# Kernel optimization log

Hardware: AMD Instinct MI355X
Metric: run time of the kernel (lower is better)

## Reference

```python
import jax, jax.numpy as jnp
import numpy as np

N, B, E, H = 16384, 16, 131072, 2
NPG = N // B  # nodes per graph
DIMS = [128, 256, 512]  # in==out channels per GAT layer


def setup_inputs() -> dict:
    key = jax.random.key(0)
    ks = iter(jax.random.split(key, 40))
    inp = {"node_feats": jax.random.normal(next(ks), (N, DIMS[0]), jnp.float32)}
    for l, d in enumerate(DIMS):
        s = 1.0 / np.sqrt(d)
        inp[f"W{l}"] = jax.random.normal(next(ks), (d, H * d), jnp.float32) * s
        inp[f"attnl{l}"] = jax.random.normal(next(ks), (H, d), jnp.float32) * 0.1
        inp[f"attnr{l}"] = jax.random.normal(next(ks), (H, d), jnp.float32) * 0.1
        inp[f"resW{l}"] = jax.random.normal(next(ks), (d, H * d), jnp.float32) * s
        inp[f"gamma{l}"] = jnp.ones((d,), jnp.float32)
        inp[f"beta{l}"] = jnp.zeros((d,), jnp.float32)
        inp[f"alpha{l}"] = jnp.ones((d,), jnp.float32)
    dst = jax.random.randint(next(ks), (E,), 0, N, jnp.int32)
    # source node sampled from the same graph as the destination
    src = (dst // NPG) * NPG + jax.random.randint(next(ks), (E,), 0, NPG, jnp.int32)
    inp["edge_src"] = src
    inp["edge_dst"] = dst
    inp["graph_ids"] = jnp.repeat(jnp.arange(B, dtype=jnp.int32), NPG)
    return inp


def _gat(x, W, al, ar, rW, src, dst, d):
    # x: [N, in]; W,rW: [in, H*d]; al,ar: [H,d]
    h = (x @ W).reshape(N, H, d)
    el = jnp.sum(h * al, -1)  # [N,H]
    er = jnp.sum(h * ar, -1)  # [N,H]
    e = jax.nn.leaky_relu(el[src] + er[dst], 0.2)  # [E,H]
    m = jax.ops.segment_max(e, dst, num_segments=N)
    ex = jnp.exp(e - m[dst])
    a = ex / jax.ops.segment_sum(ex, dst, num_segments=N)[dst]  # edge softmax
    out = jax.ops.segment_sum(h[src] * a[:, :, None], dst, num_segments=N)
    return out + (x @ rW).reshape(N, H, d)  # residual projection


def _gnorm(x, gamma, beta, alpha, eps=1e-5):
    # GraphNorm: (x - alpha*mean) / std * gamma + beta, stats over all nodes/heads
    mean = jnp.mean(x, axis=(0, 1), keepdims=True)
    sh = x - alpha * mean
    var = jnp.mean(sh * sh, axis=(0, 1), keepdims=True)
    return gamma * sh * jax.lax.rsqrt(var + eps) + beta


def reference(node_feats, W0, attnl0, attnr0, resW0, gamma0, beta0, alpha0,
              W1, attnl1, attnr1, resW1, gamma1, beta1, alpha1,
              W2, attnl2, attnr2, resW2, gamma2, beta2, alpha2,
              edge_src, edge_dst, graph_ids):
    params = [(W0, attnl0, attnr0, resW0, gamma0, beta0, alpha0),
              (W1, attnl1, attnr1, resW1, gamma1, beta1, alpha1),
              (W2, attnl2, attnr2, resW2, gamma2, beta2, alpha2)]
    counts = jax.ops.segment_sum(jnp.ones((N,), jnp.float32), graph_ids, num_segments=B)
    x = node_feats
    parts = []
    for l, d in enumerate(DIMS):
        W, al, ar, rW, g, b, a_ = params[l]
        x = _gat(x.reshape(N, -1), W, al, ar, rW, edge_src, edge_dst, d)  # [N,H,d]
        x = _gnorm(x, g, b, a_)
        x = jax.nn.leaky_relu(x, 0.01)
        nm = x.mean(1)  # [N,d] head-mean stored as 'updated_feats'
        parts.append(jax.ops.segment_sum(nm, graph_ids, num_segments=B) / counts[:, None])
    return jax.nn.leaky_relu(jnp.concatenate(parts, -1), 0.01)  # [B, 896]
```

## Files before the change

### kernel.cpp

```cpp
#include <hip/hip_runtime.h>
#include <math.h>

constexpr int NNODES  = 16384;
constexpr int NEDGES  = 131072;
constexpr int NGRAPHS = 16;

typedef short bf16x8 __attribute__((ext_vector_type(8)));
typedef short bf16x4 __attribute__((ext_vector_type(4)));
typedef float f32x4  __attribute__((ext_vector_type(4)));

__device__ __forceinline__ float leaky(float x, float s){ return x >= 0.0f ? x : s * x; }

__device__ __forceinline__ unsigned short f2bf(float f){
  unsigned u = __builtin_bit_cast(unsigned, f);
  u += 0x7FFFu + ((u >> 16) & 1u);
  return (unsigned short)(u >> 16);
}
__device__ __forceinline__ float bf2f(unsigned short u){
  unsigned x = (unsigned)u << 16; return __builtin_bit_cast(float, x);
}

__device__ __forceinline__ void gload_lds16(const unsigned short* g, unsigned short* l){
  __builtin_amdgcn_global_load_lds((const __attribute__((address_space(1))) void*)g,
                                   (__attribute__((address_space(3))) void*)l, 16, 0, 0);
}

__global__ void k_deg(const int* __restrict__ dst, int* __restrict__ deg){
  int e = blockIdx.x * 256 + threadIdx.x;
  if (e < NEDGES) atomicAdd(&deg[dst[e]], 1);
}

__global__ __launch_bounds__(1024) void k_scan(const int* __restrict__ deg,
                                               int* __restrict__ rowptr,
                                               int* __restrict__ cursor){
  __shared__ int sums[1024];
  int t = threadIdx.x;
  int loc[16];
  int s = 0;
  #pragma unroll
  for (int i = 0; i < 16; i++){ loc[i] = deg[t*16 + i]; s += loc[i]; }
  sums[t] = s; __syncthreads();
  for (int off = 1; off < 1024; off <<= 1){
    int v = (t >= off) ? sums[t - off] : 0;
    __syncthreads();
    sums[t] += v;
    __syncthreads();
  }
  int base = (t > 0) ? sums[t-1] : 0;
  #pragma unroll
  for (int i = 0; i < 16; i++){
    rowptr[t*16 + i] = base; cursor[t*16 + i] = base; base += loc[i];
  }
  if (t == 1023) rowptr[NNODES] = base;
}

__global__ void k_scatter(const int* __restrict__ src, const int* __restrict__ dst,
                          int* __restrict__ cursor, int* __restrict__ perm){
  int e = blockIdx.x * 256 + threadIdx.x;
  if (e < NEDGES){ int p = atomicAdd(&cursor[dst[e]], 1); perm[p] = src[e]; }
}

__global__ __launch_bounds__(256) void k_counts(const int* __restrict__ gid, float* __restrict__ counts){
  __shared__ int h[NGRAPHS];
  int t = threadIdx.x;
  if (t < NGRAPHS) h[t] = 0;
  __syncthreads();
  int base = blockIdx.x * 1024;
  #pragma unroll
  for (int i = 0; i < 4; i++)
    atomicAdd(&h[gid[base + t + i*256]], 1);
  __syncthreads();
  if (t < NGRAPHS && h[t] > 0) atomicAdd(&counts[t], (float)h[t]);
}

__global__ void k_cvt(const float* __restrict__ in, unsigned short* __restrict__ out, int n4){
  int i = blockIdx.x * 256 + threadIdx.x;
  if (i >= n4) return;
  float4 v = ((const float4*)in)[i];
  ushort4 o; o.x = f2bf(v.x); o.y = f2bf(v.y); o.z = f2bf(v.z); o.w = f2bf(v.w);
  ((ushort4*)out)[i] = o;
}

__global__ __launch_bounds__(256) void k_cvt_t(const float* __restrict__ W,
                                               unsigned short* __restrict__ Wt,
                                               int K, int NN){
  __shared__ float tile[32][33];
  int n0 = blockIdx.x * 32, k0 = blockIdx.y * 32;
  int tx = threadIdx.x & 31, ty = threadIdx.x >> 5;
  #pragma unroll
  for (int i = 0; i < 4; i++)
    tile[ty + i*8][tx] = W[(size_t)(k0 + ty + i*8) * NN + n0 + tx];
  __syncthreads();
  #pragma unroll
  for (int i = 0; i < 4; i++)
    Wt[(size_t)(n0 + ty + i*8) * K + k0 + tx] = f2bf(tile[tx][ty + i*8]);
}

__global__ __launch_bounds__(256) void k_gemm2(const unsigned short* __restrict__ A,
                                               const unsigned short* __restrict__ Wt,
                                               const unsigned short* __restrict__ RWt,
                                               unsigned short* __restrict__ HB,
                                               float* __restrict__ RB,
                                               int K, int NN){
  __shared__ unsigned short As[2][128 * 64];
  __shared__ unsigned short Bs[2][128 * 64];
  int t = threadIdx.x;
  int lane = t & 63, w = t >> 6;
  int nx  = gridDim.x;
  int nwg = nx * gridDim.y;
  int bid = blockIdx.x + blockIdx.y * nx;
  int wg  = (bid & 7) * (nwg >> 3) + (bid >> 3);
  int bx = wg % nx, by = wg / nx;
  int half = nx >> 1;
  bool isW = bx < half;
  const unsigned short* Bt = isW ? Wt : RWt;
  int colB = (isW ? bx : bx - half) * 128;
  int rowA = by * 128;

  int wr = (w >> 1) * 64, wc = (w & 1) * 64;
  int l16 = lane & 15, lhi = lane >> 4;
  int r8  = lane >> 3;
  int kcs = (((lane & 7) * 16) ^ (r8 << 4)) >> 1;
  f32x4 acc[4][4] = {};

  const unsigned short* Ap = A  + (size_t)(rowA) * K + kcs;
  const unsigned short* Bp = Bt + (size_t)(colB) * K + kcs;

  int nt = K >> 6;
  #pragma unroll
  for (int i = 0; i < 4; i++){
    int c = w * 4 + i;
    int row = c * 8 + r8;
    gload_lds16(Ap + (size_t)row * K, &As[0][c * 512]);
    gload_lds16(Bp + (size_t)row * K, &Bs[0][c * 512]);
  }
  __syncthreads();

  int cur = 0;
  for (int tI = 0; tI < nt; tI++){
    if (tI + 1 < nt){
      int k0n = (tI + 1) << 6;
      #pragma unroll
      for (int i = 0; i < 4; i++){
        int c = w * 4 + i;
        int row = c * 8 + r8;
        gload_lds16(Ap + (size_t)row * K + k0n, &As[cur ^ 1][c * 512]);
        gload_lds16(Bp + (size_t)row * K + k0n, &Bs[cur ^ 1][c * 512]);
      }
    }
    bf16x8 af[4][2], bfr[4][2];
    #pragma unroll
    for (int mi = 0; mi < 4; mi++){
      int row = wr + mi * 16 + l16;
      #pragma unroll
      for (int s = 0; s < 2; s++){
        int k = s * 32 + lhi * 8;
        int off = row * 128 + ((k * 2) ^ ((row & 7) << 4));
        af[mi][s] = *(const bf16x8*)((const char*)As[cur] + off);
      }
    }
    #pragma unroll
    for (int ni = 0; ni < 4; ni++){
      int row = wc + ni * 16 + l16;
      #pragma unroll
      for (int s = 0; s < 2; s++){
        int k = s * 32 + lhi * 8;
        int off = row * 128 + ((k * 2) ^ ((row & 7) << 4));
        bfr[ni][s] = *(const bf16x8*)((const char*)Bs[cur] + off);
      }
    }
    #pragma unroll
    for (int mi = 0; mi < 4; mi++)
      #pragma unroll
      for (int ni = 0; ni < 4; ni++){
        acc[mi][ni] = __builtin_amdgcn_mfma_f32_16x16x32_bf16(af[mi][0], bfr[ni][0], acc[mi][ni], 0, 0, 0);
        acc[mi][ni] = __builtin_amdgcn_mfma_f32_16x16x32_bf16(af[mi][1], bfr[ni][1], acc[mi][ni], 0, 0, 0);
      }
    __syncthreads();
    cur ^= 1;
  }

  #pragma unroll
  for (int mi = 0; mi < 4; mi++){
    #pragma unroll
    for (int j = 0; j < 4; j++){
      int r = rowA + wr + mi * 16 + lhi * 4 + j;
      if (isW){
        unsigned short* Cp = HB + (size_t)r * NN + colB + wc + l16;
        #pragma unroll
        for (int ni = 0; ni < 4; ni++)
          Cp[ni * 16] = f2bf(acc[mi][ni][j]);
      } else {
        float* Cp = RB + (size_t)r * NN + colB + wc + l16;
        #pragma unroll
        for (int ni = 0; ni < 4; ni++)
          Cp[ni * 16] = acc[mi][ni][j];
      }
    }
  }
}

template<int D>
__global__ __launch_bounds__(256) void k_elr(const unsigned short* __restrict__ HB,
                                             const float* __restrict__ al,
                                             const float* __restrict__ ar,
                                             float* __restrict__ el, float* __restrict__ er){
  constexpr int ITER = (2*D)/256;
  int wid = threadIdx.x >> 6, lane = threadIdx.x & 63;
  int n = blockIdx.x * 4 + wid;
  const unsigned short* hrow = HB + (size_t)n * (2*D);
  float sl[2] = {0.f, 0.f}, sr[2] = {0.f, 0.f};
  #pragma unroll
  for (int j = 0; j < ITER; j++){
    int base = j*256 + lane*4;
    bf16x4 v = *(const bf16x4*)(hrow + base);
    int hh = (base < D) ? 0 : 1;
    #pragma unroll
    for (int i = 0; i < 4; i++){
      float f = bf2f((unsigned short)v[i]);
      sl[hh] += f * al[base + i];
      sr[hh] += f * ar[base + i];
    }
  }
  #pragma unroll
  for (int o = 32; o; o >>= 1){
    sl[0] += __shfl_xor(sl[0], o); sl[1] += __shfl_xor(sl[1], o);
    sr[0] += __shfl_xor(sr[0], o); sr[1] += __shfl_xor(sr[1], o);
  }
  if (lane < 2){ el[n*2 + lane] = sl[lane]; er[n*2 + lane] = sr[lane]; }
}

template<int D>
__global__ __launch_bounds__(256) void k_attn(const unsigned short* __restrict__ HB,
                                              float* __restrict__ RB,
                                              const float* __restrict__ el,
                                              const float* __restrict__ er,
                                              const int* __restrict__ rowptr,
                                              const int* __restrict__ perm){
  constexpr int ITER = (2*D)/256;
  int wid = threadIdx.x >> 6, lane = threadIdx.x & 63;
  int nb = (blockIdx.x & 7) * (NNODES/4/8) + (blockIdx.x >> 3);
  int n = nb * 4 + wid;
  int r0 = rowptr[n], r1 = rowptr[n+1];
  if (r0 == r1) return;
  float er0 = er[n*2], er1 = er[n*2+1];
  float mx0 = -1e30f, mx1 = -1e30f;
  for (int e = r0 + lane; e < r1; e += 64){
    int s = perm[e];
    mx0 = fmaxf(mx0, leaky(el[s*2]   + er0, 0.2f));
    mx1 = fmaxf(mx1, leaky(el[s*2+1] + er1, 0.2f));
  }
  #pragma unroll
  for (int o = 32; o; o >>= 1){ mx0 = fmaxf(mx0, __shfl_xor(mx0, o)); mx1 = fmaxf(mx1, __shfl_xor(mx1, o)); }
  float sm0 = 0.0f, sm1 = 0.0f;
  for (int e = r0 + lane; e < r1; e += 64){
    int s = perm[e];
    sm0 += expf(leaky(el[s*2]   + er0, 0.2f) - mx0);
    sm1 += expf(leaky(el[s*2+1] + er1, 0.2f) - mx1);
  }
  #pragma unroll
  for (int o = 32; o; o >>= 1){ sm0 += __shfl_xor(sm0, o); sm1 += __shfl_xor(sm1, o); }
  float inv0 = 1.0f / sm0, inv1 = 1.0f / sm1;
  float acc[ITER][4];
  #pragma unroll
  for (int j = 0; j < ITER; j++)
    #pragma unroll
    for (int i = 0; i < 4; i++) acc[j][i] = 0.0f;
  for (int e = r0; e < r1; ++e){
    int s = perm[e];
    float a0 = expf(leaky(el[s*2]   + er0, 0.2f) - mx0) * inv0;
    float a1 = expf(leaky(el[s*2+1] + er1, 0.2f) - mx1) * inv1;
    const unsigned short* hrow = HB + (size_t)s * (2*D);
    #pragma unroll
    for (int j = 0; j < ITER; j++){
      int base = j*256 + lane*4;
      bf16x4 v = *(const bf16x4*)(hrow + base);
      float a = (base < D) ? a0 : a1;
      #pragma unroll
      for (int i = 0; i < 4; i++)
        acc[j][i] += a * bf2f((unsigned short)v[i]);
    }
  }
  float* rrow = RB + (size_t)n * (2*D);
  #pragma unroll
  for (int j = 0; j < ITER; j++){
    int base = j*256 + lane*4;
    float4 r = *(float4*)(rrow + base);
    r.x += acc[j][0]; r.y += acc[j][1]; r.z += acc[j][2]; r.w += acc[j][3];
    *(float4*)(rrow + base) = r;
  }
}

__global__ __launch_bounds__(256) void k_stats(const float* __restrict__ R, int nn,
                                               float* __restrict__ gsum, float* __restrict__ gsq){
  int t = threadIdx.x, lane = t & 63, w = t >> 6;
  int c = blockIdx.y * 256 + lane * 4;
  const float* base = R + (size_t)(blockIdx.x * 128 + w) * nn + c;
  float4 s = make_float4(0,0,0,0), q = make_float4(0,0,0,0);
  #pragma unroll 4
  for (int i = 0; i < 32; i++){
    float4 v = *(const float4*)(base + (size_t)(i * 4) * nn);
    s.x += v.x; s.y += v.y; s.z += v.z; s.w += v.w;
    q.x += v.x*v.x; q.y += v.y*v.y; q.z += v.z*v.z; q.w += v.w*v.w;
  }
  __shared__ float4 rs[256], rq[256];
  rs[t] = s; rq[t] = q; __syncthreads();
  if (t < 64){
    float4 a = rs[t], b = rs[t+64], c2 = rs[t+128], d2 = rs[t+192];
    float4 e = rq[t], f = rq[t+64], g2 = rq[t+128], h2 = rq[t+192];
    int cc = blockIdx.y * 256 + t * 4;
    atomicAdd(&gsum[cc+0], a.x+b.x+c2.x+d2.x);
    atomicAdd(&gsum[cc+1], a.y+b.y+c2.y+d2.y);
    atomicAdd(&gsum[cc+2], a.z+b.z+c2.z+d2.z);
    atomicAdd(&gsum[cc+3], a.w+b.w+c2.w+d2.w);
    atomicAdd(&gsq [cc+0], e.x+f.x+g2.x+h2.x);
    atomicAdd(&gsq [cc+1], e.y+f.y+g2.y+h2.y);
    atomicAdd(&gsq [cc+2], e.z+f.z+g2.z+h2.z);
    atomicAdd(&gsq [cc+3], e.w+f.w+g2.w+h2.w);
  }
}

__global__ void k_finstats(const float* __restrict__ gsum, const float* __restrict__ gsq,
                           const float* __restrict__ alpha,
                           float* __restrict__ mean, float* __restrict__ rstd, int d){
  int t = threadIdx.x;
  if (t >= d) return;
  float s = gsum[t] + gsum[t + d];
  float q = gsq[t]  + gsq[t + d];
  const float M = (float)(2 * NNODES);
  float m   = s / M;
  float msq = q / M;
  float a   = alpha[t];
  float var = msq - a * m * m * (2.0f - a);
  mean[t] = m;
  rstd[t] = rsqrtf(var + 1e-5f);
}

__global__ __launch_bounds__(256) void k_norm_pool(const float* __restrict__ R,
                                                   unsigned short* __restrict__ Xn,
                                                   const float* __restrict__ mean,
                                                   const float* __restrict__ rstd,
                                                   const float* __restrict__ gamma,
                                                   const float* __restrict__ beta,
                                                   const float* __restrict__ alpha,
                                                   float* __restrict__ pool, int d, int loff){
  int t = threadIdx.x, lane = t & 63, w = t >> 6;
  int c = blockIdx.y * 256 + lane * 4;
  int cm = c & (d - 1);
  int nodeb = blockIdx.x * 128;
  int g = blockIdx.x >> 3;
  int nn = 2 * d;
  float4 mm = *(const float4*)(mean + cm);
  float4 rr = *(const float4*)(rstd + cm);
  float4 gg = *(const float4*)(gamma + cm);
  float4 bb = *(const float4*)(beta + cm);
  float4 aa = *(const float4*)(alpha + cm);
  float am0 = aa.x*mm.x, am1 = aa.y*mm.y, am2 = aa.z*mm.z, am3 = aa.w*mm.w;
  const float* base = R + (size_t)(nodeb + w) * nn + c;
  unsigned short* xb = Xn ? (Xn + (size_t)(nodeb + w) * nn + c) : nullptr;
  float4 accp = make_float4(0,0,0,0);
  #pragma unroll 4
  for (int i = 0; i < 32; i++){
    float4 v = *(const float4*)(base + (size_t)(i * 4) * nn);
    float y0 = gg.x*(v.x-am0)*rr.x + bb.x; y0 = y0 >= 0.f ? y0 : 0.01f*y0;
    float y1 = gg.y*(v.y-am1)*rr.y + bb.y; y1 = y1 >= 0.f ? y1 : 0.01f*y1;
    float y2 = gg.z*(v.z-am2)*rr.z + bb.z; y2 = y2 >= 0.f ? y2 : 0.01f*y2;
    float y3 = gg.w*(v.w-am3)*rr.w + bb.w; y3 = y3 >= 0.f ? y3 : 0.01f*y3;
    if (xb){
      ushort4 o; o.x = f2bf(y0); o.y = f2bf(y1); o.z = f2bf(y2); o.w = f2bf(y3);
      *(ushort4*)(xb + (size_t)(i * 4) * nn) = o;
    }
    accp.x += y0; accp.y += y1; accp.z += y2; accp.w += y3;
  }
  __shared__ float4 red[256];
  red[t] = accp; __syncthreads();
  if (t < 64){
    float4 a = red[t], b = red[t+64], c2 = red[t+128], d2 = red[t+192];
    int cc = blockIdx.y * 256 + t * 4;
    float* pb = pool + g * 896 + loff;
    atomicAdd(&pb[(cc+0) & (d-1)], 0.5f*(a.x+b.x+c2.x+d2.x));
    atomicAdd(&pb[(cc+1) & (d-1)], 0.5f*(a.y+b.y+c2.y+d2.y));
    atomicAdd(&pb[(cc+2) & (d-1)], 0.5f*(a.z+b.z+c2.z+d2.z));
    atomicAdd(&pb[(cc+3) & (d-1)], 0.5f*(a.w+b.w+c2.w+d2.w));
  }
}

__global__ void k_final(const float* __restrict__ pool, const float* __restrict__ counts,
                        float* __restrict__ out){
  int idx = blockIdx.x * 256 + threadIdx.x;
  if (idx >= NGRAPHS * 896) return;
  int g = idx / 896;
  float v = pool[idx] / counts[g];
  out[idx] = v >= 0.0f ? v : 0.01f * v;
}

extern "C" void kernel_launch(void* const* d_in, const int* in_sizes, int n_in,
                              void* d_out, int out_size, void* d_ws, size_t ws_size,
                              hipStream_t stream){
  const float* x0 = (const float*)d_in[0];
  const float *W[3], *AL[3], *AR[3], *RW[3], *GA[3], *BE[3], *ALP[3];
  for (int l = 0; l < 3; l++){
    const int b = 1 + l*7;
    W[l]  = (const float*)d_in[b+0];
    AL[l] = (const float*)d_in[b+1];
    AR[l] = (const float*)d_in[b+2];
    RW[l] = (const float*)d_in[b+3];
    GA[l] = (const float*)d_in[b+4];
    BE[l] = (const float*)d_in[b+5];
    ALP[l]= (const float*)d_in[b+6];
  }
  const int* esrc = (const int*)d_in[22];
  const int* edst = (const int*)d_in[23];
  const int* gid  = (const int*)d_in[24];
  float* out = (float*)d_out;

  char* p = (char*)d_ws;
  auto carve = [&](size_t bytes)->void*{
    void* r = (void*)p; p += (bytes + 255) & ~(size_t)255; return r;
  };
  unsigned short* HB = (unsigned short*)carve((size_t)NNODES * 1024 * 2);
  float* RB     = (float*)carve((size_t)NNODES * 1024 * 4);
  unsigned short* X0b = (unsigned short*)carve((size_t)NNODES * 128 * 2);
  unsigned short* XA  = (unsigned short*)carve((size_t)NNODES * 256 * 2);
  unsigned short* XB  = (unsigned short*)carve((size_t)NNODES * 512 * 2);
  unsigned short* Wt  = (unsigned short*)carve((size_t)1024 * 512 * 2);
  unsigned short* RWt = (unsigned short*)carve((size_t)1024 * 512 * 2);
  float* el     = (float*)carve((size_t)NNODES * 2 * 4);
  float* er     = (float*)carve((size_t)NNODES * 2 * 4);
  int*   deg    = (int*)  carve((size_t)NNODES * 4);
  int*   rowptr = (int*)  carve((size_t)(NNODES + 1) * 4);
  int*   cursor = (int*)  carve((size_t)NNODES * 4);
  int*   perm   = (int*)  carve((size_t)NEDGES * 4);
  float* stats  = (float*)carve(2048 * 4);
  float* meanb  = (float*)carve(512 * 4);
  float* rstdb  = (float*)carve(512 * 4);
  float* pool   = (float*)carve((size_t)NGRAPHS * 896 * 4);
  float* countsF= (float*)carve((size_t)NGRAPHS * 4);
  (void)ws_size; (void)in_sizes; (void)n_in; (void)out_size;

  hipMemsetAsync(deg, 0, NNODES * 4, stream);
  hipMemsetAsync(pool, 0, NGRAPHS * 896 * 4, stream);
  hipMemsetAsync(countsF, 0, NGRAPHS * 4, stream);

  k_deg    <<<NEDGES/256, 256, 0, stream>>>(edst, deg);
  k_scan   <<<1, 1024, 0, stream>>>(deg, rowptr, cursor);
  k_scatter<<<NEDGES/256, 256, 0, stream>>>(esrc, edst, cursor, perm);
  k_counts <<<NNODES/1024, 256, 0, stream>>>(gid, countsF);
  k_cvt    <<<(NNODES*128/4 + 255)/256, 256, 0, stream>>>(x0, X0b, NNODES*128/4);

  const unsigned short* xin = X0b;
  int loff = 0;
  const int dims[3] = {128, 256, 512};
  for (int l = 0; l < 3; l++){
    int d = dims[l], nn = 2*d;
    dim3 gt(nn/32, d/32);
    k_cvt_t<<<gt, 256, 0, stream>>>(W[l],  Wt,  d, nn);
    k_cvt_t<<<gt, 256, 0, stream>>>(RW[l], RWt, d, nn);
    dim3 gg(2*nn/128, NNODES/128);
    k_gemm2<<<gg, 256, 0, stream>>>(xin, Wt, RWt, HB, RB, d, nn);
    if (d == 128){
      k_elr <128><<<NNODES/4, 256, 0, stream>>>(HB, AL[l], AR[l], el, er);
      k_attn<128><<<NNODES/4, 256, 0, stream>>>(HB, RB, el, er, rowptr, perm);
    } else if (d == 256){
      k_elr <256><<<NNODES/4, 256, 0, stream>>>(HB, AL[l], AR[l], el, er);
      k_attn<256><<<NNODES/4, 256, 0, stream>>>(HB, RB, el, er, rowptr, perm);
    } else {
      k_elr <512><<<NNODES/4, 256, 0, stream>>>(HB, AL[l], AR[l], el, er);
      k_attn<512><<<NNODES/4, 256, 0, stream>>>(HB, RB, el, er, rowptr, perm);
    }
    hipMemsetAsync(stats, 0, 2048 * 4, stream);
    dim3 gs(NNODES/128, nn/256);
    k_stats   <<<gs, 256, 0, stream>>>(RB, nn, stats, stats + 1024);
    k_finstats<<<1, 512, 0, stream>>>(stats, stats + 1024, ALP[l], meanb, rstdb, d);
    unsigned short* xn = (l == 0) ? XA : (l == 1) ? XB : nullptr;
    k_norm_pool<<<gs, 256, 0, stream>>>(RB, xn, meanb, rstdb, GA[l], BE[l], ALP[l], pool, d, loff);
    xin = xn; loff += d;
  }
  k_final<<<(NGRAPHS*896 + 255)/256, 256, 0, stream>>>(pool, countsF, out);
}
```

Measured before the change: 364.3 us.

## Fuse attention logits into GEMM epilogue and store residual buffer in bf16

Removes the separate el/er kernel by computing the per-node attention dot products in the GEMM epilogue from fp32 accumulators, reduced with lane shuffles and atomically added into zeroed el/er buffers. The residual projection buffer RB moves from fp32 to bf16, which halves its traffic in the GEMM store, the attention read-modify-write, the stats pass and the norm/pool pass. This adds atomics and memsets, and bf16 rounding of the pre-norm activations lowers accuracy.

After: 395.3 us. 1.09x slower.

```diff
diff --git a/kernel.cpp b/kernel.cpp
--- a/kernel.cpp
+++ b/kernel.cpp
@@ -100,7 +100,11 @@
                                                const unsigned short* __restrict__ Wt,
                                                const unsigned short* __restrict__ RWt,
                                                unsigned short* __restrict__ HB,
-                                               float* __restrict__ RB,
+                                               unsigned short* __restrict__ RB,
+                                               const float* __restrict__ al,
+                                               const float* __restrict__ ar,
+                                               float* __restrict__ el,
+                                               float* __restrict__ er,
                                                int K, int NN){
   __shared__ unsigned short As[2][128 * 64];
   __shared__ unsigned short Bs[2][128 * 64];
@@ -180,59 +184,52 @@
     cur ^= 1;
   }
 
+  unsigned short* C = isW ? HB : RB;
   #pragma unroll
   for (int mi = 0; mi < 4; mi++){
     #pragma unroll
     for (int j = 0; j < 4; j++){
       int r = rowA + wr + mi * 16 + lhi * 4 + j;
-      if (isW){
-        unsigned short* Cp = HB + (size_t)r * NN + colB + wc + l16;
+      unsigned short* Cp = C + (size_t)r * NN + colB + wc + l16;
+      #pragma unroll
+      for (int ni = 0; ni < 4; ni++)
+        Cp[ni * 16] = f2bf(acc[mi][ni][j]);
+    }
+  }
+
+  if (isW){
+    int hd = (colB >= (NN >> 1)) ? 1 : 0;
+    float alv[4], arv[4];
+    #pragma unroll
+    for (int ni = 0; ni < 4; ni++){
+      int col = colB + wc + ni * 16 + l16;
+      alv[ni] = al[col]; arv[ni] = ar[col];
+    }
+    #pragma unroll
+    for (int mi = 0; mi < 4; mi++){
+      #pragma unroll
+      for (int j = 0; j < 4; j++){
+        float pe = 0.f, pr = 0.f;
         #pragma unroll
-        for (int ni = 0; ni < 4; ni++)
-          Cp[ni * 16] = f2bf(acc[mi][ni][j]);
-      } else {
-        float* Cp = RB + (size_t)r * NN + colB + wc + l16;
+        for (int ni = 0; ni < 4; ni++){
+          float v = acc[mi][ni][j];
+          pe += v * alv[ni]; pr += v * arv[ni];
+        }
         #pragma unroll
-        for (int ni = 0; ni < 4; ni++)
-          Cp[ni * 16] = acc[mi][ni][j];
+        for (int o = 8; o; o >>= 1){ pe += __shfl_xor(pe, o); pr += __shfl_xor(pr, o); }
+        if (l16 == 0){
+          int r = rowA + wr + mi * 16 + lhi * 4 + j;
+          atomicAdd(&el[r * 2 + hd], pe);
+          atomicAdd(&er[r * 2 + hd], pr);
+        }
       }
     }
   }
-}
-
-template<int D>
-__global__ __launch_bounds__(256) void k_elr(const unsigned short* __restrict__ HB,
-                                             const float* __restrict__ al,
-                                             const float* __restrict__ ar,
-                                             float* __restrict__ el, float* __restrict__ er){
-  constexpr int ITER = (2*D)/256;
-  int wid = threadIdx.x >> 6, lane = threadIdx.x & 63;
-  int n = blockIdx.x * 4 + wid;
-  const unsigned short* hrow = HB + (size_t)n * (2*D);
-  float sl[2] = {0.f, 0.f}, sr[2] = {0.f, 0.f};
-  #pragma unroll
-  for (int j = 0; j < ITER; j++){
-    int base = j*256 + lane*4;
-    bf16x4 v = *(const bf16x4*)(hrow + base);
-    int hh = (base < D) ? 0 : 1;
-    #pragma unroll
-    for (int i = 0; i < 4; i++){
-      float f = bf2f((unsigned short)v[i]);
-      sl[hh] += f * al[base + i];
-      sr[hh] += f * ar[base + i];
-    }
-  }
-  #pragma unroll
-  for (int o = 32; o; o >>= 1){
-    sl[0] += __shfl_xor(sl[0], o); sl[1] += __shfl_xor(sl[1], o);
-    sr[0] += __shfl_xor(sr[0], o); sr[1] += __shfl_xor(sr[1], o);
-  }
-  if (lane < 2){ el[n*2 + lane] = sl[lane]; er[n*2 + lane] = sr[lane]; }
 }
 
 template<int D>
 __global__ __launch_bounds__(256) void k_attn(const unsigned short* __restrict__ HB,
-                                              float* __restrict__ RB,
+                                              unsigned short* __restrict__ RB,
                                               const float* __restrict__ el,
                                               const float* __restrict__ er,
                                               const int* __restrict__ rowptr,
@@ -281,27 +278,33 @@
         acc[j][i] += a * bf2f((unsigned short)v[i]);
     }
   }
-  float* rrow = RB + (size_t)n * (2*D);
+  unsigned short* rrow = RB + (size_t)n * (2*D);
   #pragma unroll
   for (int j = 0; j < ITER; j++){
     int base = j*256 + lane*4;
-    float4 r = *(float4*)(rrow + base);
-    r.x += acc[j][0]; r.y += acc[j][1]; r.z += acc[j][2]; r.w += acc[j][3];
-    *(float4*)(rrow + base) = r;
-  }
-}
-
-__global__ __launch_bounds__(256) void k_stats(const float* __restrict__ R, int nn,
+    bf16x4 r = *(bf16x4*)(rrow + base);
+    ushort4 o;
+    o.x = f2bf(bf2f((unsigned short)r[0]) + acc[j][0]);
+    o.y = f2bf(bf2f((unsigned short)r[1]) + acc[j][1]);
+    o.z = f2bf(bf2f((unsigned short)r[2]) + acc[j][2]);
+    o.w = f2bf(bf2f((unsigned short)r[3]) + acc[j][3]);
+    *(ushort4*)(rrow + base) = o;
+  }
+}
+
+__global__ __launch_bounds__(256) void k_stats(const unsigned short* __restrict__ R, int nn,
                                                float* __restrict__ gsum, float* __restrict__ gsq){
   int t = threadIdx.x, lane = t & 63, w = t >> 6;
   int c = blockIdx.y * 256 + lane * 4;
-  const float* base = R + (size_t)(blockIdx.x * 128 + w) * nn + c;
+  const unsigned short* base = R + (size_t)(blockIdx.x * 128 + w) * nn + c;
   float4 s = make_float4(0,0,0,0), q = make_float4(0,0,0,0);
   #pragma unroll 4
   for (int i = 0; i < 32; i++){
-    float4 v = *(const float4*)(base + (size_t)(i * 4) * nn);
-    s.x += v.x; s.y += v.y; s.z += v.z; s.w += v.w;
-    q.x += v.x*v.x; q.y += v.y*v.y; q.z += v.z*v.z; q.w += v.w*v.w;
+    bf16x4 bv = *(const bf16x4*)(base + (size_t)(i * 4) * nn);
+    float vx = bf2f((unsigned short)bv[0]), vy = bf2f((unsigned short)bv[1]);
+    float vz = bf2f((unsigned short)bv[2]), vw = bf2f((unsigned short)bv[3]);
+    s.x += vx; s.y += vy; s.z += vz; s.w += vw;
+    q.x += vx*vx; q.y += vy*vy; q.z += vz*vz; q.w += vw*vw;
   }
   __shared__ float4 rs[256], rq[256];
   rs[t] = s; rq[t] = q; __syncthreads();
@@ -336,7 +339,7 @@
   rstd[t] = rsqrtf(var + 1e-5f);
 }
 
-__global__ __launch_bounds__(256) void k_norm_pool(const float* __restrict__ R,
+__global__ __launch_bounds__(256) void k_norm_pool(const unsigned short* __restrict__ R,
                                                    unsigned short* __restrict__ Xn,
                                                    const float* __restrict__ mean,
                                                    const float* __restrict__ rstd,
@@ -356,16 +359,18 @@
   float4 bb = *(const float4*)(beta + cm);
   float4 aa = *(const float4*)(alpha + cm);
   float am0 = aa.x*mm.x, am1 = aa.y*mm.y, am2 = aa.z*mm.z, am3 = aa.w*mm.w;
-  const float* base = R + (size_t)(nodeb + w) * nn + c;
+  const unsigned short* base = R + (size_t)(nodeb + w) * nn + c;
   unsigned short* xb = Xn ? (Xn + (size_t)(nodeb + w) * nn + c) : nullptr;
   float4 accp = make_float4(0,0,0,0);
   #pragma unroll 4
   for (int i = 0; i < 32; i++){
-    float4 v = *(const float4*)(base + (size_t)(i * 4) * nn);
-    float y0 = gg.x*(v.x-am0)*rr.x + bb.x; y0 = y0 >= 0.f ? y0 : 0.01f*y0;
-    float y1 = gg.y*(v.y-am1)*rr.y + bb.y; y1 = y1 >= 0.f ? y1 : 0.01f*y1;
-    float y2 = gg.z*(v.z-am2)*rr.z + bb.z; y2 = y2 >= 0.f ? y2 : 0.01f*y2;
-    float y3 = gg.w*(v.w-am3)*rr.w + bb.w; y3 = y3 >= 0.f ? y3 : 0.01f*y3;
+    bf16x4 bv = *(const bf16x4*)(base + (size_t)(i * 4) * nn);
+    float vx = bf2f((unsigned short)bv[0]), vy = bf2f((unsigned short)bv[1]);
+    float vz = bf2f((unsigned short)bv[2]), vw = bf2f((unsigned short)bv[3]);
+    float y0 = gg.x*(vx-am0)*rr.x + bb.x; y0 = y0 >= 0.f ? y0 : 0.01f*y0;
+    float y1 = gg.y*(vy-am1)*rr.y + bb.y; y1 = y1 >= 0.f ? y1 : 0.01f*y1;
+    float y2 = gg.z*(vz-am2)*rr.z + bb.z; y2 = y2 >= 0.f ? y2 : 0.01f*y2;
+    float y3 = gg.w*(vw-am3)*rr.w + bb.w; y3 = y3 >= 0.f ? y3 : 0.01f*y3;
     if (xb){
       ushort4 o; o.x = f2bf(y0); o.y = f2bf(y1); o.z = f2bf(y2); o.w = f2bf(y3);
       *(ushort4*)(xb + (size_t)(i * 4) * nn) = o;
@@ -419,7 +424,7 @@
     void* r = (void*)p; p += (bytes + 255) & ~(size_t)255; return r;
   };
   unsigned short* HB = (unsigned short*)carve((size_t)NNODES * 1024 * 2);
-  float* RB     = (float*)carve((size_t)NNODES * 1024 * 4);
+  unsigned short* RB = (unsigned short*)carve((size_t)NNODES * 1024 * 2);
   unsigned short* X0b = (unsigned short*)carve((size_t)NNODES * 128 * 2);
   unsigned short* XA  = (unsigned short*)carve((size_t)NNODES * 256 * 2);
   unsigned short* XB  = (unsigned short*)carve((size_t)NNODES * 512 * 2);
@@ -456,16 +461,15 @@
     dim3 gt(nn/32, d/32);
     k_cvt_t<<<gt, 256, 0, stream>>>(W[l],  Wt,  d, nn);
     k_cvt_t<<<gt, 256, 0, stream>>>(RW[l], RWt, d, nn);
+    hipMemsetAsync(el, 0, NNODES * 2 * 4, stream);
+    hipMemsetAsync(er, 0, NNODES * 2 * 4, stream);
     dim3 gg(2*nn/128, NNODES/128);
-    k_gemm2<<<gg, 256, 0, stream>>>(xin, Wt, RWt, HB, RB, d, nn);
+    k_gemm2<<<gg, 256, 0, stream>>>(xin, Wt, RWt, HB, RB, AL[l], AR[l], el, er, d, nn);
     if (d == 128){
-      k_elr <128><<<NNODES/4, 256, 0, stream>>>(HB, AL[l], AR[l], el, er);
       k_attn<128><<<NNODES/4, 256, 0, stream>>>(HB, RB, el, er, rowptr, perm);
     } else if (d == 256){
-      k_elr <256><<<NNODES/4, 256, 0, stream>>>(HB, AL[l], AR[l], el, er);
       k_attn<256><<<NNODES/4, 256, 0, stream>>>(HB, RB, el, er, rowptr, perm);
     } else {
-      k_elr <512><<<NNODES/4, 256, 0, stream>>>(HB, AL[l], AR[l], el, er);
       k_attn<512><<<NNODES/4, 256, 0, stream>>>(HB, RB, el, er, rowptr, perm);
     }
     hipMemsetAsync(stats, 0, 2048 * 4, stream);
```
